# Kernel optimization log

Hardware: AMD Instinct MI355X
Metric: run time of the kernel (lower is better)

## Reference

```python
import jax, jax.numpy as jnp
import numpy as np

N_INV, N_FUND = 100000, 20000
D_INV, D_FUND, H = 128, 64, 128
E, EL = 600000, 200000


def setup_inputs() -> dict:
    key = jax.random.key(0)
    ks = jax.random.split(key, 26)
    f = lambda k, shape: (jax.random.normal(k, shape, dtype=jnp.float32) * 0.05)
    inp = {
        'x_inv': jax.random.normal(ks[0], (N_INV, D_INV), dtype=jnp.float32),
        'x_fund': jax.random.normal(ks[1], (N_FUND, D_FUND), dtype=jnp.float32),
        'src_if': jax.random.randint(ks[2], (E,), 0, N_INV),
        'dst_if': jax.random.randint(ks[3], (E,), 0, N_FUND),
        'src_fi': jax.random.randint(ks[4], (E,), 0, N_FUND),
        'dst_fi': jax.random.randint(ks[5], (E,), 0, N_INV),
        'eli_inv': jax.random.randint(ks[6], (EL,), 0, N_INV),
        'eli_fund': jax.random.randint(ks[7], (EL,), 0, N_FUND),
        # layer-1 SAGEConv weights per relation (PyG: out = lin_l(mean(x_j)) + lin_r(x_dst))
        'W1l_if': f(ks[8], (H, D_INV)), 'b1_if': jnp.zeros((H,), jnp.float32), 'W1r_if': f(ks[9], (H, D_FUND)),
        'W1l_fi': f(ks[10], (H, D_FUND)), 'b1_fi': jnp.zeros((H,), jnp.float32), 'W1r_fi': f(ks[11], (H, D_INV)),
        # layer-2 SAGEConv weights per relation
        'W2l_if': f(ks[12], (H, H)), 'b2_if': jnp.zeros((H,), jnp.float32), 'W2r_if': f(ks[13], (H, H)),
        'W2l_fi': f(ks[14], (H, H)), 'b2_fi': jnp.zeros((H,), jnp.float32), 'W2r_fi': f(ks[15], (H, H)),
        # link predictor MLP
        'Wp1': f(ks[16], (H, 2 * H)), 'bp1': jnp.zeros((H,), jnp.float32),
        'Wp2': f(ks[17], (1, H)), 'bp2': jnp.zeros((1,), jnp.float32),
    }
    return inp


def _sage(x_src, x_dst, src, dst, n_dst, Wl, bl, Wr):
    # mean-aggregate neighbor messages, then lin_l(mean) + bias + lin_r(root)
    msg = x_src[src]                                              # [E, d_src]
    s = jax.ops.segment_sum(msg, dst, num_segments=n_dst)         # [n_dst, d_src]
    cnt = jax.ops.segment_sum(jnp.ones((src.shape[0],), x_src.dtype), dst, num_segments=n_dst)
    mean = s / jnp.maximum(cnt, 1.0)[:, None]                     # isolated nodes -> 0
    return mean @ Wl.T + bl + x_dst @ Wr.T


def reference(x_inv, x_fund, src_if, dst_if, src_fi, dst_fi, eli_inv, eli_fund,
              W1l_if, b1_if, W1r_if, W1l_fi, b1_fi, W1r_fi,
              W2l_if, b2_if, W2r_if, W2l_fi, b2_fi, W2r_fi,
              Wp1, bp1, Wp2, bp2):
    # layer 1 (hetero: one incoming relation per node type, aggr='sum' is identity)
    h_fund = jax.nn.relu(_sage(x_inv, x_fund, src_if, dst_if, N_FUND, W1l_if, b1_if, W1r_if))
    h_inv = jax.nn.relu(_sage(x_fund, x_inv, src_fi, dst_fi, N_INV, W1l_fi, b1_fi, W1r_fi))
    # layer 2
    z_fund = _sage(h_inv, h_fund, src_if, dst_if, N_FUND, W2l_if, b2_if, W2r_if)
    z_inv = _sage(h_fund, h_inv, src_fi, dst_fi, N_INV, W2l_fi, b2_fi, W2r_fi)
    # link predictor
    xi = z_inv[eli_inv]                                           # [EL, H]
    xj = z_fund[eli_fund]                                         # [EL, H]
    x = jnp.concatenate([xi, xj], axis=-1)                        # [EL, 2H]
    x = jax.nn.relu(x @ Wp1.T + bp1)
    return jax.nn.sigmoid(x @ Wp2.T + bp2)                        # [EL, 1]
```

## Files before the change

### kernel.cpp

```cpp
#include <hip/hip_runtime.h>
#include <cstdint>
#include <cstddef>

namespace {

typedef short bf16x8 __attribute__((ext_vector_type(8)));
typedef float f32x4 __attribute__((ext_vector_type(4)));

constexpr int kNInv  = 100000;
constexpr int kNFund = 20000;
constexpr int kH     = 128;
constexpr int kE     = 600000;
constexpr int kEL    = 200000;

constexpr int kW1lIF = 0;
constexpr int kW1rIF = 16384;
constexpr int kW1lFI = 24576;
constexpr int kW1rFI = 32768;
constexpr int kWTot  = 49152;

constexpr int kCW2lFI = 0;
constexpr int kCW2rFI = 16384;
constexpr int kCW2lIF = 32768;
constexpr int kCW2rIF = 49152;

__device__ __forceinline__ float bf_lo(uint32_t u) {
  union { uint32_t i; float f; } v; v.i = u << 16; return v.f;
}
__device__ __forceinline__ float bf_hi(uint32_t u) {
  union { uint32_t i; float f; } v; v.i = u & 0xffff0000u; return v.f;
}
__device__ __forceinline__ ushort f2bf(float f) {
  union { float f; uint32_t i; } v; v.f = f;
  uint32_t x = v.i;
  return (ushort)((x + 0x7fffu + ((x >> 16) & 1u)) >> 16);
}

constexpr int kXiQ = kNInv * 128 / 4;
constexpr int kXfQ = kNFund * 64 / 4;
constexpr int kWQ  = kWTot / 4;
constexpr int kTotQ = kXiQ + kXfQ + kWQ;
constexpr int kQT  = kTotQ / 4;
constexpr int kZF4 = kNFund / 4;
constexpr int kZ4  = (kNFund + kNInv) / 16;
constexpr int kPrepT = kQT + kZ4;
constexpr int kPrepB = (kPrepT + 255) / 256;

__device__ void convert_body(int t, const float* __restrict__ xi, const float* __restrict__ xf,
                             const float* w0, const float* w1, const float* w2, const float* w3,
                             ushort* __restrict__ xi_b, ushort* __restrict__ xf_b,
                             ushort* __restrict__ wa,
                             int* __restrict__ deg_fund, int* __restrict__ deg_inv) {
  if (t >= kQT) {
    const int g = t - kQT;
    if (g >= kZ4) return;
    int z = g * 4;
#pragma unroll
    for (int j = 0; j < 4; ++j, ++z) {
      if (z < kZF4) ((int4*)deg_fund)[z] = make_int4(0, 0, 0, 0);
      else ((int4*)deg_inv)[z - kZF4] = make_int4(0, 0, 0, 0);
    }
    return;
  }
  const int q0 = t * 4;
  const float* src;
  ushort* dst;
  int sq, dq;
  if (q0 < kXiQ) {
    src = xi; dst = xi_b; sq = q0; dq = q0;
  } else if (q0 < kXiQ + kXfQ) {
    src = xf; dst = xf_b; sq = q0 - kXiQ; dq = sq;
  } else {
    const int e = (q0 - kXiQ - kXfQ) * 4;
    const float* ws[4] = {w0, w1, w2, w3};
    const int beg[5] = {kW1lIF, kW1rIF, kW1lFI, kW1rFI, kWTot};
    int s = 0;
    while (e >= beg[s + 1]) ++s;
    src = ws[s]; dst = wa; sq = (e - beg[s]) / 4; dq = e / 4;
  }
#pragma unroll
  for (int j = 0; j < 4; ++j) {
    float4 v = ((const float4*)src)[sq + j];
    ushort4 o = make_ushort4(f2bf(v.x), f2bf(v.y), f2bf(v.z), f2bf(v.w));
    ((ushort4*)dst)[dq + j] = o;
  }
}

__device__ void composite_body(int b, const float* __restrict__ Wp1,
                               const float* __restrict__ W2l_fi, const float* __restrict__ W2r_fi,
                               const float* __restrict__ W2l_if, const float* __restrict__ W2r_if,
                               const float* __restrict__ b2_fi, const float* __restrict__ b2_if,
                               const float* __restrict__ bp1,
                               ushort* __restrict__ cw, float* __restrict__ bu_inv,
                               float* __restrict__ bu_fund, float* sA ) {
  const int tid = threadIdx.x;
  if (b == 16) {
    if (tid < 128) {
      float s = 0.f;
      for (int j = 0; j < 128; ++j) s += Wp1[(size_t)tid * 256 + j] * b2_fi[j];
      bu_inv[tid] = s;
    } else {
      const int o = tid - 128;
      float s = bp1[o];
      for (int j = 0; j < 128; ++j) s += Wp1[(size_t)o * 256 + 128 + j] * b2_if[j];
      bu_fund[o] = s;
    }
    return;
  }
  const int m = b >> 2;
  const int rb = (b & 3) * 32;
  const float* A = Wp1 + (m >= 2 ? 128 : 0);
  const float* B = (m == 0) ? W2l_fi : (m == 1) ? W2r_fi : (m == 2) ? W2l_if : W2r_if;
  for (int i = tid; i < 32 * 128; i += 256) {
    const int r = i >> 7, c = i & 127;
    sA[r * 132 + c] = A[(size_t)(rb + r) * 256 + c];
  }
  __syncthreads();
  const int lr = tid >> 3;
  const int k0 = (tid & 7) * 16;
  float acc[16];
#pragma unroll
  for (int i = 0; i < 16; ++i) acc[i] = 0.f;
  for (int j = 0; j < 128; ++j) {
    const float a = sA[lr * 132 + j];
    const float* Brow = B + (size_t)j * 128 + k0;
#pragma unroll
    for (int i = 0; i < 16; i += 4) {
      float4 v = *(const float4*)(Brow + i);
      acc[i] += a * v.x; acc[i + 1] += a * v.y; acc[i + 2] += a * v.z; acc[i + 3] += a * v.w;
    }
  }
  ushort* dst = cw + (size_t)m * 16384 + (size_t)(rb + lr) * 128 + k0;
  ushort ov[16];
#pragma unroll
  for (int i = 0; i < 16; ++i) ov[i] = f2bf(acc[i]);
#pragma unroll
  for (int i = 0; i < 16; i += 4)
    *(ushort4*)(dst + i) = *(const ushort4*)(ov + i);
}

__global__ __launch_bounds__(256) void prep(
    const float* xi, const float* xf,
    const float* w0, const float* w1, const float* w2, const float* w3,
    ushort* xi_b, ushort* xf_b, ushort* wa,
    int* deg_fund, int* deg_inv,
    const float* Wp1, const float* W2l_fi, const float* W2r_fi,
    const float* W2l_if, const float* W2r_if,
    const float* b2_fi, const float* b2_if, const float* bp1,
    ushort* cw, float* bu_inv, float* bu_fund) {
  __shared__ float smem[32 * 132];
  const int b = blockIdx.x;
  if (b < kPrepB) {
    convert_body(b * 256 + threadIdx.x, xi, xf, w0, w1, w2, w3, xi_b, xf_b, wa,
                 deg_fund, deg_inv);
  } else {
    composite_body(b - kPrepB, Wp1, W2l_fi, W2r_fi, W2l_if, W2r_if,
                   b2_fi, b2_if, bp1, cw, bu_inv, bu_fund, smem);
  }
}

__global__ void count_rank2(const int* __restrict__ d0, int* __restrict__ g0,
                            int* __restrict__ r0v,
                            const int* __restrict__ d1, int* __restrict__ g1,
                            int* __restrict__ r1v, int n4) {
  const int t = blockIdx.x * blockDim.x + threadIdx.x;
  if (t < n4) {
    int4 d = ((const int4*)d0)[t];
    const int e = t * 4;
    r0v[e]     = atomicAdd(&g0[d.x], 1);
    r0v[e + 1] = atomicAdd(&g0[d.y], 1);
    r0v[e + 2] = atomicAdd(&g0[d.z], 1);
    r0v[e + 3] = atomicAdd(&g0[d.w], 1);
  } else if (t < 2 * n4) {
    const int tt = t - n4;
    int4 d = ((const int4*)d1)[tt];
    const int e = tt * 4;
    r1v[e]     = atomicAdd(&g1[d.x], 1);
    r1v[e + 1] = atomicAdd(&g1[d.y], 1);
    r1v[e + 2] = atomicAdd(&g1[d.z], 1);
    r1v[e + 3] = atomicAdd(&g1[d.w], 1);
  }
}


__device__ __forceinline__ void scan_partial_body(const int* __restrict__ deg,
                                                  int* __restrict__ bsum, int n, int blk) {
  __shared__ int red[256];
  const int tid = threadIdx.x;
  const int base = blk * 1024 + tid * 4;
  int s = 0;
  if (base + 3 < n) {
    int4 v = *(const int4*)(deg + base);
    s = v.x + v.y + v.z + v.w;
  } else {
    for (int i = 0; i < 4; ++i)
      if (base + i < n) s += deg[base + i];
  }
  red[tid] = s;
  __syncthreads();
  for (int d = 128; d > 0; d >>= 1) {
    if (tid < d) red[tid] += red[tid + d];
    __syncthreads();
  }
  if (tid == 0) bsum[blk] = red[0];
}

__global__ void scan_partial2(const int* __restrict__ degF, int* __restrict__ bsumF, int nF, int nbF,
                              const int* __restrict__ degI, int* __restrict__ bsumI, int nI) {
  if ((int)blockIdx.x < nbF) scan_partial_body(degF, bsumF, nF, blockIdx.x);
  else scan_partial_body(degI, bsumI, nI, blockIdx.x - nbF);
}

__device__ __forceinline__ void scan_apply_body(const int* __restrict__ deg,
                                                const int* __restrict__ bsum,
                                                int* __restrict__ off, int n, int blk) {
  __shared__ int red[256];
  __shared__ int sbase;
  const int tid = threadIdx.x;
  int part = 0;
  for (int i = tid; i < blk; i += 256) part += bsum[i];
  red[tid] = part;
  __syncthreads();
  for (int d = 128; d > 0; d >>= 1) {
    if (tid < d) red[tid] += red[tid + d];
    __syncthreads();
  }
  if (tid == 0) sbase = red[0];
  __syncthreads();
  const int base0 = sbase;
  __syncthreads();

  const int base = blk * 1024 + tid * 4;
  int v[4] = {0, 0, 0, 0};
  const bool full = (base + 3 < n);
  if (full) {
    int4 t = *(const int4*)(deg + base);
    v[0] = t.x; v[1] = t.y; v[2] = t.z; v[3] = t.w;
  } else {
    for (int i = 0; i < 4; ++i)
      if (base + i < n) v[i] = deg[base + i];
  }
  const int s = v[0] + v[1] + v[2] + v[3];
  red[tid] = s;
  __syncthreads();
  for (int d = 1; d < 256; d <<= 1) {
    int t = (tid >= d) ? red[tid - d] : 0;
    __syncthreads();
    red[tid] += t;
    __syncthreads();
  }
  int o[4];
  o[0] = base0 + red[tid] - s;
  o[1] = o[0] + v[0];
  o[2] = o[1] + v[1];
  o[3] = o[2] + v[2];
  if (full) {
    *(int4*)(off + base) = make_int4(o[0], o[1], o[2], o[3]);
  } else {
    for (int i = 0; i < 4; ++i)
      if (base + i < n) off[base + i] = o[i];
  }
#pragma unroll
  for (int i = 0; i < 4; ++i)
    if (base + i == n - 1) off[n] = o[i] + v[i];
}

__global__ void scan_apply2(const int* __restrict__ degF, const int* __restrict__ bsumF,
                            int* __restrict__ offF, int nF, int nbF,
                            const int* __restrict__ degI, const int* __restrict__ bsumI,
                            int* __restrict__ offI, int nI) {
  if ((int)blockIdx.x < nbF) scan_apply_body(degF, bsumF, offF, nF, blockIdx.x);
  else scan_apply_body(degI, bsumI, offI, nI, blockIdx.x - nbF);
}

__global__ void fill2(const int* __restrict__ s0, const int* __restrict__ d0,
                      const int* __restrict__ r0v, const int* __restrict__ off0,
                      int* __restrict__ c0,
                      const int* __restrict__ s1, const int* __restrict__ d1,
                      const int* __restrict__ r1v, const int* __restrict__ off1,
                      int* __restrict__ c1, int n) {
  int e = blockIdx.x * blockDim.x + threadIdx.x;
  if (e < n) {
    c0[off0[d0[e]] + r0v[e]] = s0[e];
  } else if (e < 2 * n) {
    int ee = e - n;
    c1[off1[d1[ee]] + r1v[ee]] = s1[ee];
  }
}


__device__ __forceinline__ void acc8w(float* a, uint4 u, float w) {
  a[0] = fmaf(w, bf_lo(u.x), a[0]); a[1] = fmaf(w, bf_hi(u.x), a[1]);
  a[2] = fmaf(w, bf_lo(u.y), a[2]); a[3] = fmaf(w, bf_hi(u.y), a[3]);
  a[4] = fmaf(w, bf_lo(u.z), a[4]); a[5] = fmaf(w, bf_hi(u.z), a[5]);
  a[6] = fmaf(w, bf_lo(u.w), a[6]); a[7] = fmaf(w, bf_hi(u.w), a[7]);
}

template <int D, int DEP>
__device__ __forceinline__ void mean_node(const ushort* __restrict__ xsrc,
                                          const int* __restrict__ csr,
                                          const int* __restrict__ off,
                                          ushort* __restrict__ mean, int node, int lane) {
  constexpr int NSUB = (D == 128) ? 4 : 8;
  const int sub = (D == 128) ? (lane >> 4) : (lane >> 3);
  const int ll  = (D == 128) ? (lane & 15) : (lane & 7);
  const size_t co = (size_t)ll * 8;
  const int lo = off[node], hi = off[node + 1];
  float a[8] = {0.f, 0.f, 0.f, 0.f, 0.f, 0.f, 0.f, 0.f};
  for (int e0 = lo + sub; e0 < hi; e0 += NSUB * DEP) {
    int idx[DEP];
    float w[DEP];
#pragma unroll
    for (int j = 0; j < DEP; ++j) {
      const int e = e0 + NSUB * j;
      idx[j] = csr[min(e, hi - 1)];
      w[j] = (e < hi) ? 1.0f : 0.0f;
    }
    uint4 u[DEP];
#pragma unroll
    for (int j = 0; j < DEP; ++j)
      u[j] = *(const uint4*)(xsrc + (size_t)idx[j] * D + co);
#pragma unroll
    for (int j = 0; j < DEP; ++j) acc8w(a, u[j], w[j]);
  }
#pragma unroll
  for (int i = 0; i < 8; ++i) {
    if (D == 64) a[i] += __shfl_xor(a[i], 8);
    a[i] += __shfl_xor(a[i], 16);
    a[i] += __shfl_xor(a[i], 32);
  }
  if (sub == 0) {
    const float sc = (hi > lo) ? 1.0f / (float)(hi - lo) : 0.0f;
    ushort o8[8];
#pragma unroll
    for (int i = 0; i < 8; ++i) o8[i] = f2bf(a[i] * sc);
    *(uint4*)(mean + (size_t)node * D + co) = *(const uint4*)o8;
  }
}

template <int DA, int DEPA, int DB, int DEPB>
__global__ void sage_mean_dual(const ushort* __restrict__ xA, const int* __restrict__ csrA,
                               const int* __restrict__ offA, ushort* __restrict__ outA, int nA,
                               const ushort* __restrict__ xB, const int* __restrict__ csrB,
                               const int* __restrict__ offB, ushort* __restrict__ outB, int nB) {
  const int wave = (int)((blockIdx.x * blockDim.x + threadIdx.x) >> 6);
  const int lane = threadIdx.x & 63;
  if (wave < nA) mean_node<DA, DEPA>(xA, csrA, offA, outA, wave, lane);
  else if (wave < nA + nB) mean_node<DB, DEPB>(xB, csrB, offB, outB, wave - nA, lane);
}


template <int D1, int D2>
__device__ void gemm_body(const ushort* __restrict__ A1, const ushort* __restrict__ A2,
                          const ushort* __restrict__ W1, const ushort* __restrict__ W2,
                          const float* __restrict__ bias, int act,
                          ushort* __restrict__ out, int n, int blk, ushort* lds) {
  constexpr int K1 = D1 / 32;
  constexpr int K2 = D2 / 32;
  constexpr int CH1 = 128 * D1 / 8;
  constexpr int CHT = 128 * (D1 + D2) / 8;

  const int tid = threadIdx.x;
  const int wid = tid >> 6;
  const int lane = tid & 63;
  const int lo16 = lane & 15;
  const int hi4 = lane >> 4;
  const int row0 = blk * 128 + wid * 32;

  const int r0 = min(row0 + lo16, n - 1);
  const int r1 = min(row0 + 16 + lo16, n - 1);

  bf16x8 aA[2][K1], aB[2][K2];
  {
    const ushort* a0p = A1 + (size_t)r0 * D1 + hi4 * 8;
    const ushort* a1p = A1 + (size_t)r1 * D1 + hi4 * 8;
#pragma unroll
    for (int k = 0; k < K1; ++k) {
      aA[0][k] = *(const bf16x8*)(a0p + k * 32);
      aA[1][k] = *(const bf16x8*)(a1p + k * 32);
    }
    const ushort* b0p = A2 + (size_t)r0 * D2 + hi4 * 8;
    const ushort* b1p = A2 + (size_t)r1 * D2 + hi4 * 8;
#pragma unroll
    for (int k = 0; k < K2; ++k) {
      aB[0][k] = *(const bf16x8*)(b0p + k * 32);
      aB[1][k] = *(const bf16x8*)(b1p + k * 32);
    }
  }

#pragma unroll
  for (int it = 0; it < CHT / 256; ++it) {
    const int c = it * 256 + tid;
    const int g = c * 8;
    bf16x8 v;
    int dest;
    if (g < 128 * D1) {
      const int row = g / D1, col = g % D1;
      v = *(const bf16x8*)(W1 + g);
      dest = ((col >> 5) * 8 + (row >> 4)) * 64 + (((col >> 3) & 3) << 4) + (row & 15);
    } else {
      const int g2 = g - 128 * D1;
      const int row = g2 / D2, col = g2 % D2;
      v = *(const bf16x8*)(W2 + g2);
      dest = CH1 + ((col >> 5) * 8 + (row >> 4)) * 64 + (((col >> 3) & 3) << 4) + (row & 15);
    }
    *((bf16x8*)lds + dest) = v;
  }
  __syncthreads();

  f32x4 acc[2][8];
#pragma unroll
  for (int rt = 0; rt < 2; ++rt)
#pragma unroll
    for (int ct = 0; ct < 8; ++ct)
      acc[rt][ct] = (f32x4){0.f, 0.f, 0.f, 0.f};

  const bf16x8* fr = (const bf16x8*)lds;
#pragma unroll
  for (int k = 0; k < K1; ++k) {
#pragma unroll
    for (int ct = 0; ct < 8; ++ct) {
      bf16x8 w = fr[(k * 8 + ct) * 64 + lane];
      acc[0][ct] = __builtin_amdgcn_mfma_f32_16x16x32_bf16(w, aA[0][k], acc[0][ct], 0, 0, 0);
      acc[1][ct] = __builtin_amdgcn_mfma_f32_16x16x32_bf16(w, aA[1][k], acc[1][ct], 0, 0, 0);
    }
  }
#pragma unroll
  for (int k = 0; k < K2; ++k) {
#pragma unroll
    for (int ct = 0; ct < 8; ++ct) {
      bf16x8 w = fr[CH1 + (k * 8 + ct) * 64 + lane];
      acc[0][ct] = __builtin_amdgcn_mfma_f32_16x16x32_bf16(w, aB[0][k], acc[0][ct], 0, 0, 0);
      acc[1][ct] = __builtin_amdgcn_mfma_f32_16x16x32_bf16(w, aB[1][k], acc[1][ct], 0, 0, 0);
    }
  }

  const int colb = hi4 * 4;
#pragma unroll
  for (int rt = 0; rt < 2; ++rt) {
    const int row = row0 + rt * 16 + lo16;
    if (row < n) {
#pragma unroll
      for (int ct = 0; ct < 8; ++ct) {
        float b4[4];
        *(float4*)b4 = *(const float4*)(bias + ct * 16 + colb);
        ushort o[4];
#pragma unroll
        for (int j = 0; j < 4; ++j) {
          float x = acc[rt][ct][j] + b4[j];
          if (act) x = fmaxf(x, 0.f);
          o[j] = f2bf(x);
        }
        *(ushort4*)(out + (size_t)row * kH + ct * 16 + colb) = *(const ushort4*)o;
      }
    }
  }
}

__global__ __launch_bounds__(256) void gemm_stage1(
    const ushort* A1f, const ushort* A2f, const ushort* W1f, const ushort* W2f,
    const float* biasf, ushort* outf, int nf, int nbf,
    const ushort* A1i, const ushort* A2i, const ushort* W1i, const ushort* W2i,
    const float* biasi, ushort* outi, int ni) {
  __shared__ ushort lds[128 * 192];
  if ((int)blockIdx.x < nbf)
    gemm_body<128, 64>(A1f, A2f, W1f, W2f, biasf, 1, outf, nf, blockIdx.x, lds);
  else
    gemm_body<64, 128>(A1i, A2i, W1i, W2i, biasi, 1, outi, ni, blockIdx.x - nbf, lds);
}

__global__ __launch_bounds__(256) void gemm_stage2(
    const ushort* A1f, const ushort* A2f, const ushort* W1f, const ushort* W2f,
    const float* biasf, ushort* outf, int nf, int nbf,
    const ushort* A1i, const ushort* A2i, const ushort* W1i, const ushort* W2i,
    const float* biasi, ushort* outi, int ni) {
  __shared__ ushort lds[128 * 256];
  if ((int)blockIdx.x < nbf)
    gemm_body<128, 128>(A1f, A2f, W1f, W2f, biasf, 0, outf, nf, blockIdx.x, lds);
  else
    gemm_body<128, 128>(A1i, A2i, W1i, W2i, biasi, 0, outi, ni, blockIdx.x - nbf, lds);
}


__global__ void link_pred(const ushort* __restrict__ u_inv, const ushort* __restrict__ u_fund,
                          const int* __restrict__ ei, const int* __restrict__ ej,
                          const float* __restrict__ Wp2, const float* __restrict__ bp2,
                          float* __restrict__ out, int nl) {
  const int wave = (int)((blockIdx.x * blockDim.x + threadIdx.x) >> 6);
  const int lane = threadIdx.x & 63;
  const int q = lane >> 4, l16 = lane & 15;
  const int link = wave * 4 + q;
  if (link >= nl) return;
  const int i = ei[link];
  const int j = ej[link];
  uint4 ua = *(const uint4*)(u_inv + (size_t)i * 128 + l16 * 8);
  uint4 ub = *(const uint4*)(u_fund + (size_t)j * 128 + l16 * 8);
  float4 w0 = *(const float4*)(Wp2 + l16 * 8);
  float4 w1 = *(const float4*)(Wp2 + l16 * 8 + 4);
  float p = fmaxf(bf_lo(ua.x) + bf_lo(ub.x), 0.f) * w0.x
          + fmaxf(bf_hi(ua.x) + bf_hi(ub.x), 0.f) * w0.y
          + fmaxf(bf_lo(ua.y) + bf_lo(ub.y), 0.f) * w0.z
          + fmaxf(bf_hi(ua.y) + bf_hi(ub.y), 0.f) * w0.w
          + fmaxf(bf_lo(ua.z) + bf_lo(ub.z), 0.f) * w1.x
          + fmaxf(bf_hi(ua.z) + bf_hi(ub.z), 0.f) * w1.y
          + fmaxf(bf_lo(ua.w) + bf_lo(ub.w), 0.f) * w1.z
          + fmaxf(bf_hi(ua.w) + bf_hi(ub.w), 0.f) * w1.w;
#pragma unroll
  for (int o = 8; o > 0; o >>= 1) p += __shfl_xor(p, o);
  if (l16 == 0) out[link] = 1.0f / (1.0f + expf(-(p + bp2[0])));
}

}

extern "C" void kernel_launch(void* const* d_in, const int* in_sizes, int n_in,
                              void* d_out, int out_size, void* d_ws, size_t ws_size,
                              hipStream_t stream) {
  const float* x_inv  = (const float*)d_in[0];
  const float* x_fund = (const float*)d_in[1];
  const int* src_if   = (const int*)d_in[2];
  const int* dst_if   = (const int*)d_in[3];
  const int* src_fi   = (const int*)d_in[4];
  const int* dst_fi   = (const int*)d_in[5];
  const int* eli_inv  = (const int*)d_in[6];
  const int* eli_fund = (const int*)d_in[7];
  const float* W1l_if = (const float*)d_in[8];
  const float* b1_if  = (const float*)d_in[9];
  const float* W1r_if = (const float*)d_in[10];
  const float* W1l_fi = (const float*)d_in[11];
  const float* b1_fi  = (const float*)d_in[12];
  const float* W1r_fi = (const float*)d_in[13];
  const float* W2l_if = (const float*)d_in[14];
  const float* b2_if  = (const float*)d_in[15];
  const float* W2r_if = (const float*)d_in[16];
  const float* W2l_fi = (const float*)d_in[17];
  const float* b2_fi  = (const float*)d_in[18];
  const float* W2r_fi = (const float*)d_in[19];
  const float* Wp1    = (const float*)d_in[20];
  const float* bp1    = (const float*)d_in[21];
  const float* Wp2    = (const float*)d_in[22];
  const float* bp2    = (const float*)d_in[23];
  float* out = (float*)d_out;

  char* p = (char*)d_ws;
  auto alloc = [&](size_t bytes) -> void* {
    void* r = (void*)p;
    p += (bytes + 255) & ~(size_t)255;
    return r;
  };
  int* deg_fund = (int*)alloc((size_t)kNFund * 4);
  int* deg_inv  = (int*)alloc((size_t)kNInv * 4);
  int* off_fund = (int*)alloc((size_t)(kNFund + 1) * 4);
  int* off_inv  = (int*)alloc((size_t)(kNInv + 1) * 4);
  int* bsumF    = (int*)alloc((size_t)1024 * 4);
  int* bsumI    = (int*)alloc((size_t)1024 * 4);
  int* rank_if  = (int*)alloc((size_t)kE * 4);
  int* rank_fi  = (int*)alloc((size_t)kE * 4);
  int* csr_if   = (int*)alloc((size_t)kE * 4);
  int* csr_fi   = (int*)alloc((size_t)kE * 4);
  ushort* xi_b = (ushort*)alloc((size_t)kNInv * 128 * 2);
  ushort* xf_b = (ushort*)alloc((size_t)kNFund * 64 * 2);
  ushort* wa   = (ushort*)alloc((size_t)kWTot * 2);
  ushort* cw   = (ushort*)alloc((size_t)4 * 16384 * 2);
  float* bu_inv  = (float*)alloc((size_t)128 * 4);
  float* bu_fund = (float*)alloc((size_t)128 * 4);
  ushort* bufA = (ushort*)alloc((size_t)kNFund * 128 * 2);
  ushort* bufB = (ushort*)alloc((size_t)kNFund * 128 * 2);
  ushort* bufC = (ushort*)alloc((size_t)kNInv * 128 * 2);
  ushort* bufD = (ushort*)alloc((size_t)kNInv * 128 * 2);
  ushort* bufE = (ushort*)alloc((size_t)kNFund * 128 * 2);
  ushort* bufF = (ushort*)alloc((size_t)kNInv * 128 * 2);

  const int TB = 256;
  const int nbFund = (kNFund + 1023) / 1024;
  const int nbInv  = (kNInv + 1023) / 1024;
  const int gemmF = (kNFund + 127) / 128;
  const int gemmI = (kNInv + 127) / 128;

  prep<<<kPrepB + 17, 256, 0, stream>>>(
      x_inv, x_fund, W1l_if, W1r_if, W1l_fi, W1r_fi, xi_b, xf_b, wa,
      deg_fund, deg_inv,
      Wp1, W2l_fi, W2r_fi, W2l_if, W2r_if, b2_fi, b2_if, bp1, cw, bu_inv, bu_fund);

  const int n4 = kE / 4;
  count_rank2<<<(2 * n4 + TB - 1) / TB, TB, 0, stream>>>(
      dst_if, deg_fund, rank_if, dst_fi, deg_inv, rank_fi, n4);

  scan_partial2<<<nbFund + nbInv, 256, 0, stream>>>(deg_fund, bsumF, kNFund, nbFund,
                                                    deg_inv, bsumI, kNInv);
  scan_apply2<<<nbFund + nbInv, 256, 0, stream>>>(deg_fund, bsumF, off_fund, kNFund, nbFund,
                                                  deg_inv, bsumI, off_inv, kNInv);

  fill2<<<(2 * kE + TB - 1) / TB, TB, 0, stream>>>(
      src_if, dst_if, rank_if, off_fund, csr_if,
      src_fi, dst_fi, rank_fi, off_inv, csr_fi, kE);

  const int meanBlocks = (kNFund + kNInv + 3) / 4;

  sage_mean_dual<128, 4, 64, 2><<<meanBlocks, 256, 0, stream>>>(
      xi_b, csr_if, off_fund, bufA, kNFund, xf_b, csr_fi, off_inv, bufC, kNInv);
  gemm_stage1<<<gemmF + gemmI, 256, 0, stream>>>(
      bufA, xf_b, wa + kW1lIF, wa + kW1rIF, b1_if, bufB, kNFund, gemmF,
      bufC, xi_b, wa + kW1lFI, wa + kW1rFI, b1_fi, bufD, kNInv);
  sage_mean_dual<128, 4, 128, 2><<<meanBlocks, 256, 0, stream>>>(
      bufD, csr_if, off_fund, bufA, kNFund, bufB, csr_fi, off_inv, bufC, kNInv);
  gemm_stage2<<<gemmF + gemmI, 256, 0, stream>>>(
      bufA, bufB, cw + kCW2lIF, cw + kCW2rIF, bu_fund, bufE, kNFund, gemmF,
      bufC, bufD, cw + kCW2lFI, cw + kCW2rFI, bu_inv, bufF, kNInv);
  link_pred<<<(kEL / 4 + 3) / 4, 256, 0, stream>>>(bufF, bufE, eli_inv, eli_fund,
                                                   Wp2, bp2, out, kEL);
}
```

Measured before the change: 299.3 us.

## Fuse scan kernels, vectorize CSR fill, and double GEMM block rows

Merges the two-pass prefix scan into one kernel in which each block re-sums all preceding degree entries itself, removing a launch and the block-sum buffer at the cost of redundant reads. The CSR fill kernel now handles four edges per thread with int4 loads. The GEMM kernels move to 512-thread blocks covering 256 rows each, so every block loads the weight tile into LDS once for twice as many rows. The redundant prefix reads grow with block index, and larger GEMM blocks reduce the number of blocks available to fill the device.

```diff
diff --git a/kernel.cpp b/kernel.cpp
--- a/kernel.cpp
+++ b/kernel.cpp
@@ -183,42 +183,18 @@
 }
 
 
-__device__ __forceinline__ void scan_partial_body(const int* __restrict__ deg,
-                                                  int* __restrict__ bsum, int n, int blk) {
-  __shared__ int red[256];
-  const int tid = threadIdx.x;
-  const int base = blk * 1024 + tid * 4;
-  int s = 0;
-  if (base + 3 < n) {
-    int4 v = *(const int4*)(deg + base);
-    s = v.x + v.y + v.z + v.w;
-  } else {
-    for (int i = 0; i < 4; ++i)
-      if (base + i < n) s += deg[base + i];
-  }
-  red[tid] = s;
-  __syncthreads();
-  for (int d = 128; d > 0; d >>= 1) {
-    if (tid < d) red[tid] += red[tid + d];
-    __syncthreads();
-  }
-  if (tid == 0) bsum[blk] = red[0];
-}
-
-__global__ void scan_partial2(const int* __restrict__ degF, int* __restrict__ bsumF, int nF, int nbF,
-                              const int* __restrict__ degI, int* __restrict__ bsumI, int nI) {
-  if ((int)blockIdx.x < nbF) scan_partial_body(degF, bsumF, nF, blockIdx.x);
-  else scan_partial_body(degI, bsumI, nI, blockIdx.x - nbF);
-}
-
-__device__ __forceinline__ void scan_apply_body(const int* __restrict__ deg,
-                                                const int* __restrict__ bsum,
-                                                int* __restrict__ off, int n, int blk) {
+__device__ void scan_fused_body(const int* __restrict__ deg, int* __restrict__ off,
+                                int n, int blk) {
   __shared__ int red[256];
   __shared__ int sbase;
   const int tid = threadIdx.x;
   int part = 0;
-  for (int i = tid; i < blk; i += 256) part += bsum[i];
+  const int preq = (blk * 1024) / 4;
+  const int4* d4 = (const int4*)deg;
+  for (int i = tid; i < preq; i += 256) {
+    int4 v = d4[i];
+    part += v.x + v.y + v.z + v.w;
+  }
   red[tid] = part;
   __syncthreads();
   for (int d = 128; d > 0; d >>= 1) {
@@ -228,7 +204,6 @@
   if (tid == 0) sbase = red[0];
   __syncthreads();
   const int base0 = sbase;
-  __syncthreads();
 
   const int base = blk * 1024 + tid * 4;
   int v[4] = {0, 0, 0, 0};
@@ -241,6 +216,7 @@
       if (base + i < n) v[i] = deg[base + i];
   }
   const int s = v[0] + v[1] + v[2] + v[3];
+  __syncthreads();
   red[tid] = s;
   __syncthreads();
   for (int d = 1; d < 256; d <<= 1) {
@@ -265,12 +241,10 @@
     if (base + i == n - 1) off[n] = o[i] + v[i];
 }
 
-__global__ void scan_apply2(const int* __restrict__ degF, const int* __restrict__ bsumF,
-                            int* __restrict__ offF, int nF, int nbF,
-                            const int* __restrict__ degI, const int* __restrict__ bsumI,
-                            int* __restrict__ offI, int nI) {
-  if ((int)blockIdx.x < nbF) scan_apply_body(degF, bsumF, offF, nF, blockIdx.x);
-  else scan_apply_body(degI, bsumI, offI, nI, blockIdx.x - nbF);
+__global__ void scan_fused2(const int* __restrict__ degF, int* __restrict__ offF, int nF, int nbF,
+                            const int* __restrict__ degI, int* __restrict__ offI, int nI) {
+  if ((int)blockIdx.x < nbF) scan_fused_body(degF, offF, nF, blockIdx.x);
+  else scan_fused_body(degI, offI, nI, blockIdx.x - nbF);
 }
 
 __global__ void fill2(const int* __restrict__ s0, const int* __restrict__ d0,
@@ -278,13 +252,25 @@
                       int* __restrict__ c0,
                       const int* __restrict__ s1, const int* __restrict__ d1,
                       const int* __restrict__ r1v, const int* __restrict__ off1,
-                      int* __restrict__ c1, int n) {
-  int e = blockIdx.x * blockDim.x + threadIdx.x;
-  if (e < n) {
-    c0[off0[d0[e]] + r0v[e]] = s0[e];
-  } else if (e < 2 * n) {
-    int ee = e - n;
-    c1[off1[d1[ee]] + r1v[ee]] = s1[ee];
+                      int* __restrict__ c1, int n4) {
+  const int t = blockIdx.x * blockDim.x + threadIdx.x;
+  if (t < n4) {
+    int4 d = ((const int4*)d0)[t];
+    int4 r = ((const int4*)r0v)[t];
+    int4 s = ((const int4*)s0)[t];
+    c0[off0[d.x] + r.x] = s.x;
+    c0[off0[d.y] + r.y] = s.y;
+    c0[off0[d.z] + r.z] = s.z;
+    c0[off0[d.w] + r.w] = s.w;
+  } else if (t < 2 * n4) {
+    const int tt = t - n4;
+    int4 d = ((const int4*)d1)[tt];
+    int4 r = ((const int4*)r1v)[tt];
+    int4 s = ((const int4*)s1)[tt];
+    c1[off1[d.x] + r.x] = s.x;
+    c1[off1[d.y] + r.y] = s.y;
+    c1[off1[d.z] + r.z] = s.z;
+    c1[off1[d.w] + r.w] = s.w;
   }
 }
 
@@ -365,7 +351,7 @@
   const int lane = tid & 63;
   const int lo16 = lane & 15;
   const int hi4 = lane >> 4;
-  const int row0 = blk * 128 + wid * 32;
+  const int row0 = blk * 256 + wid * 32;
 
   const int r0 = min(row0 + lo16, n - 1);
   const int r1 = min(row0 + 16 + lo16, n - 1);
@@ -389,8 +375,8 @@
   }
 
 #pragma unroll
-  for (int it = 0; it < CHT / 256; ++it) {
-    const int c = it * 256 + tid;
+  for (int it = 0; it < CHT / 512; ++it) {
+    const int c = it * 512 + tid;
     const int g = c * 8;
     bf16x8 v;
     int dest;
@@ -457,7 +443,7 @@
   }
 }
 
-__global__ __launch_bounds__(256) void gemm_stage1(
+__global__ __launch_bounds__(512) void gemm_stage1(
     const ushort* A1f, const ushort* A2f, const ushort* W1f, const ushort* W2f,
     const float* biasf, ushort* outf, int nf, int nbf,
     const ushort* A1i, const ushort* A2i, const ushort* W1i, const ushort* W2i,
@@ -469,7 +455,7 @@
     gemm_body<64, 128>(A1i, A2i, W1i, W2i, biasi, 1, outi, ni, blockIdx.x - nbf, lds);
 }
 
-__global__ __launch_bounds__(256) void gemm_stage2(
+__global__ __launch_bounds__(512) void gemm_stage2(
     const ushort* A1f, const ushort* A2f, const ushort* W1f, const ushort* W2f,
     const float* biasf, ushort* outf, int nf, int nbf,
     const ushort* A1i, const ushort* A2i, const ushort* W1i, const ushort* W2i,
@@ -551,8 +537,6 @@
   int* deg_inv  = (int*)alloc((size_t)kNInv * 4);
   int* off_fund = (int*)alloc((size_t)(kNFund + 1) * 4);
   int* off_inv  = (int*)alloc((size_t)(kNInv + 1) * 4);
-  int* bsumF    = (int*)alloc((size_t)1024 * 4);
-  int* bsumI    = (int*)alloc((size_t)1024 * 4);
   int* rank_if  = (int*)alloc((size_t)kE * 4);
   int* rank_fi  = (int*)alloc((size_t)kE * 4);
   int* csr_if   = (int*)alloc((size_t)kE * 4);
@@ -573,8 +557,8 @@
   const int TB = 256;
   const int nbFund = (kNFund + 1023) / 1024;
   const int nbInv  = (kNInv + 1023) / 1024;
-  const int gemmF = (kNFund + 127) / 128;
-  const int gemmI = (kNInv + 127) / 128;
+  const int gemmF = (kNFund + 255) / 256;
+  const int gemmI = (kNInv + 255) / 256;
 
   prep<<<kPrepB + 17, 256, 0, stream>>>(
       x_inv, x_fund, W1l_if, W1r_if, W1l_fi, W1r_fi, xi_b, xf_b, wa,
@@ -585,25 +569,23 @@
   count_rank2<<<(2 * n4 + TB - 1) / TB, TB, 0, stream>>>(
       dst_if, deg_fund, rank_if, dst_fi, deg_inv, rank_fi, n4);
 
-  scan_partial2<<<nbFund + nbInv, 256, 0, stream>>>(deg_fund, bsumF, kNFund, nbFund,
-                                                    deg_inv, bsumI, kNInv);
-  scan_apply2<<<nbFund + nbInv, 256, 0, stream>>>(deg_fund, bsumF, off_fund, kNFund, nbFund,
-                                                  deg_inv, bsumI, off_inv, kNInv);
-
-  fill2<<<(2 * kE + TB - 1) / TB, TB, 0, stream>>>(
+  scan_fused2<<<nbFund + nbInv, 256, 0, stream>>>(deg_fund, off_fund, kNFund, nbFund,
+                                                  deg_inv, off_inv, kNInv);
+
+  fill2<<<(2 * n4 + TB - 1) / TB, TB, 0, stream>>>(
       src_if, dst_if, rank_if, off_fund, csr_if,
-      src_fi, dst_fi, rank_fi, off_inv, csr_fi, kE);
+      src_fi, dst_fi, rank_fi, off_inv, csr_fi, n4);
 
   const int meanBlocks = (kNFund + kNInv + 3) / 4;
 
   sage_mean_dual<128, 4, 64, 2><<<meanBlocks, 256, 0, stream>>>(
       xi_b, csr_if, off_fund, bufA, kNFund, xf_b, csr_fi, off_inv, bufC, kNInv);
-  gemm_stage1<<<gemmF + gemmI, 256, 0, stream>>>(
+  gemm_stage1<<<gemmF + gemmI, 512, 0, stream>>>(
       bufA, xf_b, wa + kW1lIF, wa + kW1rIF, b1_if, bufB, kNFund, gemmF,
       bufC, xi_b, wa + kW1lFI, wa + kW1rFI, b1_fi, bufD, kNInv);
   sage_mean_dual<128, 4, 128, 2><<<meanBlocks, 256, 0, stream>>>(
       bufD, csr_if, off_fund, bufA, kNFund, bufB, csr_fi, off_inv, bufC, kNInv);
-  gemm_stage2<<<gemmF + gemmI, 256, 0, stream>>>(
+  gemm_stage2<<<gemmF + gemmI, 512, 0, stream>>>(
       bufA, bufB, cw + kCW2lIF, cw + kCW2rIF, bu_fund, bufE, kNFund, gemmF,
       bufC, bufD, cw + kCW2lFI, cw + kCW2rFI, bu_inv, bufF, kNInv);
   link_pred<<<(kEL / 4 + 3) / 4, 256, 0, stream>>>(bufF, bufE, eli_inv, eli_fund,
```

After: 296.9 us. Within noise of the previous version (-0.8%).
